# Kernel tuning notes

Hardware: AMD Instinct MI355X
Metric: run time of the kernel (lower is better)

The kernel has to match this reference:

```python
import jax, jax.numpy as jnp
import numpy as np

IN_C = 256
ATTN_C = IN_C // 8
B, H, W = 4, 64, 64


def setup_inputs() -> dict:
    key = jax.random.key(0)
    ks = jax.random.split(key, 8)
    x = jax.random.normal(ks[0], (B, IN_C, W, H), dtype=jnp.float32)
    # 1x1 convs == channel-mixing matmuls: weight [out_c, in_c], bias [out_c]
    sq = 1.0 / np.sqrt(IN_C)
    Wq = jax.random.normal(ks[1], (ATTN_C, IN_C), dtype=jnp.float32) * sq
    bq = jnp.zeros((ATTN_C,), dtype=jnp.float32)
    Wk = jax.random.normal(ks[2], (ATTN_C, IN_C), dtype=jnp.float32) * sq
    bk = jnp.zeros((ATTN_C,), dtype=jnp.float32)
    Wv = jax.random.normal(ks[3], (IN_C, IN_C), dtype=jnp.float32) * sq
    bv = jnp.zeros((IN_C,), dtype=jnp.float32)
    # gamma initialized to zeros in the torch module; use a nonzero value so
    # the attention path contributes to the output/gradients.
    gamma = jnp.full((1,), 0.5, dtype=jnp.float32)
    return {"x": x, "Wq": Wq, "bq": bq, "Wk": Wk, "bk": bk,
            "Wv": Wv, "bv": bv, "gamma": gamma}


def reference(x, Wq, bq, Wk, bk, Wv, bv, gamma):
    bs, c, w, h = x.shape
    n = w * h
    xf = x.reshape(bs, c, n)                                   # [B, C, N]
    q = jnp.einsum('ac,bcn->ban', Wq, xf) + bq[:, None]        # [B, A, N]
    k = jnp.einsum('ac,bcn->ban', Wk, xf) + bk[:, None]        # [B, A, N]
    v = jnp.einsum('oc,bcn->bon', Wv, xf) + bv[:, None]        # [B, C, N]
    # energy = query.transpose(1,2) @ key  -> energy[b,i,j] = sum_a q[b,a,i] k[b,a,j]
    energy = jnp.einsum('bai,baj->bij', q, k)                  # [B, N, N]
    # non-standard: softmax over dim=1 (the query/i axis)
    attn = jax.nn.softmax(energy, axis=1)
    # out = value @ attn.transpose(1,2) -> out[b,c,i] = sum_j v[b,c,j] attn[b,i,j]
    out = jnp.einsum('bcj,bij->bci', v, attn)                  # [B, C, N]
    out = out.reshape(bs, c, w, h)
    return gamma * out + x
```

## Files before the change

kernel.cpp:

```cpp
#include <hip/hip_runtime.h>

#define NBATCH 4
#define CIN 256
#define CATT 32
#define NPIX 4096

static constexpr float LOG2E_F = 1.4426950408889634f;

typedef __attribute__((ext_vector_type(8))) short bf16x8;
typedef __attribute__((ext_vector_type(4))) float f32x4;

__device__ __forceinline__ unsigned short f2bf_rne(float f) {
    unsigned u = __builtin_bit_cast(unsigned, f);
    return (unsigned short)((u + 0x7fffu + ((u >> 16) & 1u)) >> 16);
}
__device__ __forceinline__ float bf2f(unsigned short h) {
    unsigned u = (unsigned)h << 16;
    return __builtin_bit_cast(float, u);
}
__device__ __forceinline__ void split8(const float* p, bf16x8& hi, bf16x8& lo) {
    const float4 a = *reinterpret_cast<const float4*>(p);
    const float4 b = *reinterpret_cast<const float4*>(p + 4);
    const float f[8] = {a.x, a.y, a.z, a.w, b.x, b.y, b.z, b.w};
    #pragma unroll
    for (int e = 0; e < 8; ++e) {
        const unsigned short h = f2bf_rne(f[e]);
        hi[e] = (short)h;
        lo[e] = (short)f2bf_rne(f[e] - bf2f(h));
    }
}
__device__ __forceinline__ bf16x8 cvt8(const float* p) {
    const float4 a = *reinterpret_cast<const float4*>(p);
    const float4 b = *reinterpret_cast<const float4*>(p + 4);
    const float f[8] = {a.x, a.y, a.z, a.w, b.x, b.y, b.z, b.w};
    bf16x8 r;
    #pragma unroll
    for (int e = 0; e < 8; ++e) r[e] = (short)f2bf_rne(f[e]);
    return r;
}
__device__ __forceinline__ void gl_lds16(const unsigned short* g, unsigned short* l) {
    __builtin_amdgcn_global_load_lds(
        (const __attribute__((address_space(1))) unsigned int*)g,
        (__attribute__((address_space(3))) unsigned int*)l, 16, 0, 0);
}

__global__ __launch_bounds__(256, 2)
void transpose_kernel(const float* __restrict__ x, unsigned short* __restrict__ xT)
{
    __shared__ unsigned short sT[64][68];
    const int t = threadIdx.x;
    const int nblk = blockIdx.x * 64;
    const int cblk = blockIdx.y * 64;
    const int b = blockIdx.z;
    const float* xb = x + ((size_t)b * CIN + cblk) * NPIX + nblk;
    const int lc = t >> 2, ln = (t & 3) << 4;
    #pragma unroll
    for (int u = 0; u < 4; ++u) {
        const float4 v = *reinterpret_cast<const float4*>(&xb[(size_t)lc * NPIX + ln + 4 * u]);
        sT[ln + 4 * u + 0][lc] = f2bf_rne(v.x);
        sT[ln + 4 * u + 1][lc] = f2bf_rne(v.y);
        sT[ln + 4 * u + 2][lc] = f2bf_rne(v.z);
        sT[ln + 4 * u + 3][lc] = f2bf_rne(v.w);
    }
    __syncthreads();
    const int rn = t >> 2, cs = (t & 3) << 4;
    const uint2 d0 = *reinterpret_cast<const uint2*>(&sT[rn][cs + 0]);
    const uint2 d1 = *reinterpret_cast<const uint2*>(&sT[rn][cs + 4]);
    const uint2 d2 = *reinterpret_cast<const uint2*>(&sT[rn][cs + 8]);
    const uint2 d3 = *reinterpret_cast<const uint2*>(&sT[rn][cs + 12]);
    unsigned short* dst = xT + ((size_t)b * NPIX + nblk + rn) * CIN + cblk + cs;
    *reinterpret_cast<uint4*>(dst)     = make_uint4(d0.x, d0.y, d1.x, d1.y);
    *reinterpret_cast<uint4*>(dst + 8) = make_uint4(d2.x, d2.y, d3.x, d3.y);
}

__global__ __launch_bounds__(256, 2)
void proj_qk_kernel(const float* __restrict__ Wq, const float* __restrict__ bq,
                    const float* __restrict__ Wk, const float* __restrict__ bk,
                    const unsigned short* __restrict__ xT,
                    unsigned short* __restrict__ qt, unsigned short* __restrict__ kt)
{
    const int t = threadIdx.x, w = t >> 6, l = t & 63, lr = l & 15, lg = l >> 4;
    const int b = blockIdx.y;
    const int n0 = blockIdx.x * 64 + 16 * w;
    const unsigned short* xrow = xT + ((size_t)b * NPIX + n0 + lr) * CIN + lg * 8;
    f32x4 aq[2] = {{0.f,0.f,0.f,0.f},{0.f,0.f,0.f,0.f}};
    f32x4 ak2[2] = {{0.f,0.f,0.f,0.f},{0.f,0.f,0.f,0.f}};
    #pragma unroll
    for (int ks = 0; ks < 8; ++ks) {
        const int ko = ks * 32 + lg * 8;
        const bf16x8 bx = *reinterpret_cast<const bf16x8*>(xrow + ks * 32);
        #pragma unroll
        for (int mt = 0; mt < 2; ++mt) {
            bf16x8 wh, wl;
            split8(&Wq[(size_t)(mt * 16 + lr) * CIN + ko], wh, wl);
            aq[mt] = __builtin_amdgcn_mfma_f32_16x16x32_bf16(wh, bx, aq[mt], 0, 0, 0);
            aq[mt] = __builtin_amdgcn_mfma_f32_16x16x32_bf16(wl, bx, aq[mt], 0, 0, 0);
            split8(&Wk[(size_t)(mt * 16 + lr) * CIN + ko], wh, wl);
            ak2[mt] = __builtin_amdgcn_mfma_f32_16x16x32_bf16(wh, bx, ak2[mt], 0, 0, 0);
            ak2[mt] = __builtin_amdgcn_mfma_f32_16x16x32_bf16(wl, bx, ak2[mt], 0, 0, 0);
        }
    }
    #pragma unroll
    for (int mt = 0; mt < 2; ++mt) {
        const float4 b4q = *reinterpret_cast<const float4*>(&bq[16 * mt + (lg << 2)]);
        const float4 b4k = *reinterpret_cast<const float4*>(&bk[16 * mt + (lg << 2)]);
        ushort4 uq, uk;
        uq.x = f2bf_rne(LOG2E_F * (aq[mt][0] + b4q.x));
        uq.y = f2bf_rne(LOG2E_F * (aq[mt][1] + b4q.y));
        uq.z = f2bf_rne(LOG2E_F * (aq[mt][2] + b4q.z));
        uq.w = f2bf_rne(LOG2E_F * (aq[mt][3] + b4q.w));
        uk.x = f2bf_rne(ak2[mt][0] + b4k.x);
        uk.y = f2bf_rne(ak2[mt][1] + b4k.y);
        uk.z = f2bf_rne(ak2[mt][2] + b4k.z);
        uk.w = f2bf_rne(ak2[mt][3] + b4k.w);
        const size_t base = ((size_t)b * NPIX + n0 + lr) * CATT + 16 * mt + (lg << 2);
        *reinterpret_cast<ushort4*>(&qt[base]) = uq;
        *reinterpret_cast<ushort4*>(&kt[base]) = uk;
    }
}

__global__ __launch_bounds__(256, 2)
void stats_kernel(const unsigned short* __restrict__ qt,
                  const unsigned short* __restrict__ kt, float* __restrict__ rs)
{
    __shared__ float sred[4][16];
    const int n = blockIdx.x;
    const int b = n & 3;
    const int jblk = (n >> 2) * 32;
    const int t = threadIdx.x, w = t >> 6, l = t & 63, lr = l & 15, lg = l >> 4;
    const int jsl = w & 1;
    const int ih = w >> 1;
    const unsigned short* qb = qt + (size_t)b * NPIX * CATT;
    const unsigned short* kb = kt + (size_t)b * NPIX * CATT;

    const bf16x8 kfrag = *reinterpret_cast<const bf16x8*>(
        &kb[(size_t)(jblk + 16 * jsl + lr) * CATT + lg * 8]);
    const f32x4 zero = {0.f, 0.f, 0.f, 0.f};
    const unsigned short* qp = qb + (size_t)(ih * 2048 + lr) * CATT + lg * 8;

    float s0 = 0.f, s1 = 0.f, s2 = 0.f, s3 = 0.f;
    bf16x8 qc0 = *reinterpret_cast<const bf16x8*>(qp);
    bf16x8 qc1 = *reinterpret_cast<const bf16x8*>(qp + 16 * CATT);
    bf16x8 qc2 = *reinterpret_cast<const bf16x8*>(qp + 32 * CATT);
    bf16x8 qc3 = *reinterpret_cast<const bf16x8*>(qp + 48 * CATT);

    for (int ib = 0; ib < 2048; ib += 64) {
        bf16x8 qn0, qn1, qn2, qn3;
        const bool more = (ib + 64) < 2048;
        if (more) {
            const unsigned short* q2 = qp + (size_t)(ib + 64) * CATT;
            qn0 = *reinterpret_cast<const bf16x8*>(q2);
            qn1 = *reinterpret_cast<const bf16x8*>(q2 + 16 * CATT);
            qn2 = *reinterpret_cast<const bf16x8*>(q2 + 32 * CATT);
            qn3 = *reinterpret_cast<const bf16x8*>(q2 + 48 * CATT);
        }
        f32x4 d;
        d = __builtin_amdgcn_mfma_f32_16x16x32_bf16(kfrag, qc0, zero, 0, 0, 0);
        s0 += __builtin_amdgcn_exp2f(d[0]); s1 += __builtin_amdgcn_exp2f(d[1]);
        s2 += __builtin_amdgcn_exp2f(d[2]); s3 += __builtin_amdgcn_exp2f(d[3]);
        d = __builtin_amdgcn_mfma_f32_16x16x32_bf16(kfrag, qc1, zero, 0, 0, 0);
        s0 += __builtin_amdgcn_exp2f(d[0]); s1 += __builtin_amdgcn_exp2f(d[1]);
        s2 += __builtin_amdgcn_exp2f(d[2]); s3 += __builtin_amdgcn_exp2f(d[3]);
        d = __builtin_amdgcn_mfma_f32_16x16x32_bf16(kfrag, qc2, zero, 0, 0, 0);
        s0 += __builtin_amdgcn_exp2f(d[0]); s1 += __builtin_amdgcn_exp2f(d[1]);
        s2 += __builtin_amdgcn_exp2f(d[2]); s3 += __builtin_amdgcn_exp2f(d[3]);
        d = __builtin_amdgcn_mfma_f32_16x16x32_bf16(kfrag, qc3, zero, 0, 0, 0);
        s0 += __builtin_amdgcn_exp2f(d[0]); s1 += __builtin_amdgcn_exp2f(d[1]);
        s2 += __builtin_amdgcn_exp2f(d[2]); s3 += __builtin_amdgcn_exp2f(d[3]);
        if (more) { qc0 = qn0; qc1 = qn1; qc2 = qn2; qc3 = qn3; }
    }
    #pragma unroll
    for (int m = 1; m < 16; m <<= 1) {
        s0 += __shfl_xor(s0, m); s1 += __shfl_xor(s1, m);
        s2 += __shfl_xor(s2, m); s3 += __shfl_xor(s3, m);
    }
    if (lr == 0) {
        sred[w][(lg << 2) + 0] = s0;
        sred[w][(lg << 2) + 1] = s1;
        sred[w][(lg << 2) + 2] = s2;
        sred[w][(lg << 2) + 3] = s3;
    }
    __syncthreads();
    if (t < 32) {
        const int j16 = t & 15, js = t >> 4;
        const float s = sred[js][j16] + sred[js + 2][j16];
        rs[(size_t)b * NPIX + jblk + t] = 1.0f / s;
    }
}

__global__ __launch_bounds__(256, 2)
void proj_v_kernel(const float* __restrict__ Wv, const float* __restrict__ bv,
                   const unsigned short* __restrict__ xT, const float* __restrict__ rs,
                   const float* __restrict__ gamma, unsigned short* __restrict__ vt)
{
    const int t = threadIdx.x, w = t >> 6, l = t & 63, lr = l & 15, lg = l >> 4;
    const int b = blockIdx.y;
    const int n0 = blockIdx.x * 32;
    const int cb = 64 * w;
    const unsigned short* xa = xT + ((size_t)b * NPIX + n0) * CIN;
    f32x4 acc[2][4] = {};
    #pragma unroll
    for (int ks = 0; ks < 8; ++ks) {
        const int ko = ks * 32 + lg * 8;
        bf16x8 af[2];
        #pragma unroll
        for (int mt = 0; mt < 2; ++mt)
            af[mt] = *reinterpret_cast<const bf16x8*>(&xa[(size_t)(16 * mt + lr) * CIN + ko]);
        #pragma unroll
        for (int ct = 0; ct < 4; ++ct) {
            const bf16x8 wf = cvt8(&Wv[(size_t)(cb + 16 * ct + lr) * CIN + ko]);
            #pragma unroll
            for (int mt = 0; mt < 2; ++mt)
                acc[mt][ct] = __builtin_amdgcn_mfma_f32_16x16x32_bf16(af[mt], wf, acc[mt][ct], 0, 0, 0);
        }
    }
    const float gv = gamma[0];
    #pragma unroll
    for (int mt = 0; mt < 2; ++mt) {
        const int nr = n0 + 16 * mt + (lg << 2);
        const float4 rs4 = *reinterpret_cast<const float4*>(&rs[(size_t)b * NPIX + nr]);
        #pragma unroll
        for (int ct = 0; ct < 4; ++ct) {
            const int c = cb + 16 * ct + lr;
            const float bb = bv[c];
            ushort4 u;
            u.x = f2bf_rne(gv * rs4.x * (acc[mt][ct][0] + bb));
            u.y = f2bf_rne(gv * rs4.y * (acc[mt][ct][1] + bb));
            u.z = f2bf_rne(gv * rs4.z * (acc[mt][ct][2] + bb));
            u.w = f2bf_rne(gv * rs4.w * (acc[mt][ct][3] + bb));
            *reinterpret_cast<ushort4*>(&vt[((size_t)b * CIN + c) * NPIX + nr]) = u;
        }
    }
}

__global__ __launch_bounds__(256, 2)
void out_kernel(const unsigned short* __restrict__ qt,
                const unsigned short* __restrict__ kt,
                const unsigned short* __restrict__ vt,
                const float* __restrict__ x, float* __restrict__ out)
{
    __shared__ unsigned short sV[3][128 * 64];
    __shared__ unsigned short sK[2][64 * 32];
    __shared__ unsigned short sPl[2][64 * 64];
    const int n = blockIdx.x;
    const int b = n & 3;
    const int rest = n >> 2;
    const int ch = rest & 1;
    const int it = rest >> 1;
    const int iblk = it * 64;
    const int cblk = ch * 128;
    const int t = threadIdx.x, w = t >> 6, l = t & 63, lr = l & 15, lg = l >> 4;
    const unsigned short* qb = qt + (size_t)b * NPIX * CATT;
    const unsigned short* kb = kt + (size_t)b * NPIX * CATT;
    const unsigned short* vb = vt + (size_t)b * CIN * NPIX;
    const f32x4 zero = {0.f, 0.f, 0.f, 0.f};

    bf16x8 qfrag[4];
    #pragma unroll
    for (int nt = 0; nt < 4; ++nt)
        qfrag[nt] = *reinterpret_cast<const bf16x8*>(
            &qb[(size_t)(iblk + 16 * nt + lr) * CATT + lg * 8]);

    const unsigned short* vsrcq[4];
    #pragma unroll
    for (int q = 0; q < 4; ++q) {
        const int r = (4 * w + q) * 8 + (l >> 3);
        const int p = l & 7;
        vsrcq[q] = vb + (size_t)(cblk + r) * NPIX + ((p ^ (r & 7)) * 8);
    }
    const int rk = w * 16 + (l >> 2);
    const unsigned short* ksrc0 = kb + (size_t)rk * CATT + (((l & 3) ^ (rk & 3)) * 8);

    const int krow = 16 * w + lr;
    const int kbyte = krow * 64 + ((lg * 16) ^ ((krow & 3) << 4));
    const int cl0 = 32 * w + lr;
    const int cl1 = cl0 + 16;
    int vbyte[2][2];
    #pragma unroll
    for (int kk = 0; kk < 2; ++kk) {
        vbyte[0][kk] = cl0 * 128 + ((kk * 64 + lg * 16) ^ ((cl0 & 7) << 4));
        vbyte[1][kk] = cl1 * 128 + ((kk * 64 + lg * 16) ^ ((cl1 & 7) << 4));
    }
    const int swz = (lr & 7) << 4;
    const int wb0 = lr * 128 + (((16 * w + 4 * lg) * 2) ^ swz);
    const int rb_col0 = (16 * lg) ^ swz;
    const int rb_col1 = (64 + 16 * lg) ^ swz;

    f32x4 acc[2][4] = {};

    #pragma unroll
    for (int q = 0; q < 4; ++q) gl_lds16(vsrcq[q], &sV[0][(4 * w + q) * 512]);
    gl_lds16(ksrc0, &sK[0][w * 512]);
    __syncthreads();

    int vs_cur = 0;
    for (int jb = 0; jb < 64; ++jb) {
        const int vs_next = (vs_cur == 2) ? 0 : vs_cur + 1;
        const int vs_prev = (vs_cur == 0) ? 2 : vs_cur - 1;
        if (jb < 63) {
            const int jn = (jb + 1) * 64;
            #pragma unroll
            for (int q = 0; q < 4; ++q)
                gl_lds16(vsrcq[q] + jn, &sV[vs_next][(4 * w + q) * 512]);
            gl_lds16(ksrc0 + (size_t)jn * CATT, &sK[(jb + 1) & 1][w * 512]);
        }
        {
            const char* skp = reinterpret_cast<const char*>(&sK[jb & 1][0]);
            const bf16x8 kf = *reinterpret_cast<const bf16x8*>(skp + kbyte);
            char* spw = reinterpret_cast<char*>(&sPl[jb & 1][0]);
            #pragma unroll
            for (int nt = 0; nt < 4; ++nt) {
                const f32x4 e = __builtin_amdgcn_mfma_f32_16x16x32_bf16(kf, qfrag[nt], zero, 0, 0, 0);
                const float p0 = __builtin_amdgcn_exp2f(e[0]);
                const float p1 = __builtin_amdgcn_exp2f(e[1]);
                const float p2 = __builtin_amdgcn_exp2f(e[2]);
                const float p3 = __builtin_amdgcn_exp2f(e[3]);
                unsigned w0, w1;
                asm("v_cvt_pk_bf16_f32 %0, %1, %2" : "=v"(w0) : "v"(p0), "v"(p1));
                asm("v_cvt_pk_bf16_f32 %0, %1, %2" : "=v"(w1) : "v"(p2), "v"(p3));
                *reinterpret_cast<uint2*>(spw + wb0 + nt * 2048) = make_uint2(w0, w1);
            }
        }
        if (jb > 0) {
            const char* spr = reinterpret_cast<const char*>(&sPl[(jb - 1) & 1][0]);
            const char* svp = reinterpret_cast<const char*>(&sV[vs_prev][0]);
            #pragma unroll
            for (int kk = 0; kk < 2; ++kk) {
                const int rbc = (kk == 0) ? rb_col0 : rb_col1;
                bf16x8 pf[4];
                #pragma unroll
                for (int nt = 0; nt < 4; ++nt)
                    pf[nt] = *reinterpret_cast<const bf16x8*>(spr + lr * 128 + nt * 2048 + rbc);
                const bf16x8 v0 = *reinterpret_cast<const bf16x8*>(svp + vbyte[0][kk]);
                const bf16x8 v1 = *reinterpret_cast<const bf16x8*>(svp + vbyte[1][kk]);
                __builtin_amdgcn_s_setprio(1);
                #pragma unroll
                for (int nt = 0; nt < 4; ++nt) {
                    acc[0][nt] = __builtin_amdgcn_mfma_f32_16x16x32_bf16(v0, pf[nt], acc[0][nt], 0, 0, 0);
                    acc[1][nt] = __builtin_amdgcn_mfma_f32_16x16x32_bf16(v1, pf[nt], acc[1][nt], 0, 0, 0);
                }
                __builtin_amdgcn_s_setprio(0);
            }
        }
        __syncthreads();
        vs_cur = vs_next;
    }
    {
        const int vs_prev = (vs_cur == 0) ? 2 : vs_cur - 1;
        const char* spr = reinterpret_cast<const char*>(&sPl[1][0]);
        const char* svp = reinterpret_cast<const char*>(&sV[vs_prev][0]);
        #pragma unroll
        for (int kk = 0; kk < 2; ++kk) {
            const int rbc = (kk == 0) ? rb_col0 : rb_col1;
            bf16x8 pf[4];
            #pragma unroll
            for (int nt = 0; nt < 4; ++nt)
                pf[nt] = *reinterpret_cast<const bf16x8*>(spr + lr * 128 + nt * 2048 + rbc);
            const bf16x8 v0 = *reinterpret_cast<const bf16x8*>(svp + vbyte[0][kk]);
            const bf16x8 v1 = *reinterpret_cast<const bf16x8*>(svp + vbyte[1][kk]);
            #pragma unroll
            for (int nt = 0; nt < 4; ++nt) {
                acc[0][nt] = __builtin_amdgcn_mfma_f32_16x16x32_bf16(v0, pf[nt], acc[0][nt], 0, 0, 0);
                acc[1][nt] = __builtin_amdgcn_mfma_f32_16x16x32_bf16(v1, pf[nt], acc[1][nt], 0, 0, 0);
            }
        }
    }

    const float* xb = x + (size_t)b * CIN * NPIX;
    float* ob = out + (size_t)b * CIN * NPIX;
    #pragma unroll
    for (int mt = 0; mt < 2; ++mt)
        #pragma unroll
        for (int nt = 0; nt < 4; ++nt)
            #pragma unroll
            for (int r = 0; r < 4; ++r) {
                const int c = cblk + 32 * w + 16 * mt + (lg << 2) + r;
                const size_t idx = (size_t)c * NPIX + iblk + 16 * nt + lr;
                ob[idx] = acc[mt][nt][r] + xb[idx];
            }
}

extern "C" void kernel_launch(void* const* d_in, const int* in_sizes, int n_in,
                              void* d_out, int out_size, void* d_ws, size_t ws_size,
                              hipStream_t stream)
{
    const float* x     = (const float*)d_in[0];
    const float* Wq    = (const float*)d_in[1];
    const float* bq    = (const float*)d_in[2];
    const float* Wk    = (const float*)d_in[3];
    const float* bk    = (const float*)d_in[4];
    const float* Wv    = (const float*)d_in[5];
    const float* bv    = (const float*)d_in[6];
    const float* gamma = (const float*)d_in[7];
    float* out = (float*)d_out;

    unsigned short* xT = (unsigned short*)d_ws;
    unsigned short* qt = xT + (size_t)NBATCH * NPIX * CIN;
    unsigned short* kt = qt + (size_t)NBATCH * NPIX * CATT;
    unsigned short* vt = kt + (size_t)NBATCH * NPIX * CATT;
    float* rsw = (float*)(vt + (size_t)NBATCH * CIN * NPIX);

    transpose_kernel<<<dim3(NPIX / 64, CIN / 64, NBATCH), 256, 0, stream>>>(x, xT);
    proj_qk_kernel<<<dim3(NPIX / 64, NBATCH), 256, 0, stream>>>(Wq, bq, Wk, bk, xT, qt, kt);
    stats_kernel<<<dim3((NPIX / 32) * NBATCH), 256, 0, stream>>>(qt, kt, rsw);
    proj_v_kernel<<<dim3(NPIX / 32, NBATCH), 256, 0, stream>>>(Wv, bv, xT, rsw, gamma, vt);
    out_kernel<<<dim3((NPIX / 64) * 2 * NBATCH), 256, 0, stream>>>(qt, kt, vt, x, out);
}
```

Before: 128.3 us.

## Fuse Q/K/V projections into one kernel and apply softmax reciprocal in attention loop

Merges the QK and V projection kernels into a single launch: two waves compute Q/K for a 32-pixel tile while all four waves compute V. Because V no longer depends on the column-softmax normalizer, the reciprocal sums are applied to the exponentiated probabilities inside the attention loop instead. This saves one kernel launch and one pass over xT, at the cost of extra multiplies and a per-iteration global load of the normalizers in the hot loop, plus an unbalanced wave workload in the fused projection.

New measurement: 129.1 us. No clear change (+0.6%).

```diff
diff --git a/kernel.cpp b/kernel.cpp
--- a/kernel.cpp
+++ b/kernel.cpp
@@ -74,48 +74,90 @@
 }
 
 __global__ __launch_bounds__(256, 2)
-void proj_qk_kernel(const float* __restrict__ Wq, const float* __restrict__ bq,
-                    const float* __restrict__ Wk, const float* __restrict__ bk,
-                    const unsigned short* __restrict__ xT,
-                    unsigned short* __restrict__ qt, unsigned short* __restrict__ kt)
+void proj_fused_kernel(const float* __restrict__ Wq, const float* __restrict__ bq,
+                       const float* __restrict__ Wk, const float* __restrict__ bk,
+                       const float* __restrict__ Wv, const float* __restrict__ bv,
+                       const float* __restrict__ gamma,
+                       const unsigned short* __restrict__ xT,
+                       unsigned short* __restrict__ qt, unsigned short* __restrict__ kt,
+                       unsigned short* __restrict__ vt)
 {
     const int t = threadIdx.x, w = t >> 6, l = t & 63, lr = l & 15, lg = l >> 4;
     const int b = blockIdx.y;
-    const int n0 = blockIdx.x * 64 + 16 * w;
-    const unsigned short* xrow = xT + ((size_t)b * NPIX + n0 + lr) * CIN + lg * 8;
-    f32x4 aq[2] = {{0.f,0.f,0.f,0.f},{0.f,0.f,0.f,0.f}};
-    f32x4 ak2[2] = {{0.f,0.f,0.f,0.f},{0.f,0.f,0.f,0.f}};
+    const int n0 = blockIdx.x * 32;
+
+    if (w < 2) {
+        const int nq = n0 + 16 * w;
+        const unsigned short* xrow = xT + ((size_t)b * NPIX + nq + lr) * CIN + lg * 8;
+        f32x4 aq[2] = {{0.f,0.f,0.f,0.f},{0.f,0.f,0.f,0.f}};
+        f32x4 ak2[2] = {{0.f,0.f,0.f,0.f},{0.f,0.f,0.f,0.f}};
+        #pragma unroll
+        for (int ks = 0; ks < 8; ++ks) {
+            const int ko = ks * 32 + lg * 8;
+            const bf16x8 bx = *reinterpret_cast<const bf16x8*>(xrow + ks * 32);
+            #pragma unroll
+            for (int mt = 0; mt < 2; ++mt) {
+                bf16x8 wh, wl;
+                split8(&Wq[(size_t)(mt * 16 + lr) * CIN + ko], wh, wl);
+                aq[mt] = __builtin_amdgcn_mfma_f32_16x16x32_bf16(wh, bx, aq[mt], 0, 0, 0);
+                aq[mt] = __builtin_amdgcn_mfma_f32_16x16x32_bf16(wl, bx, aq[mt], 0, 0, 0);
+                split8(&Wk[(size_t)(mt * 16 + lr) * CIN + ko], wh, wl);
+                ak2[mt] = __builtin_amdgcn_mfma_f32_16x16x32_bf16(wh, bx, ak2[mt], 0, 0, 0);
+                ak2[mt] = __builtin_amdgcn_mfma_f32_16x16x32_bf16(wl, bx, ak2[mt], 0, 0, 0);
+            }
+        }
+        #pragma unroll
+        for (int mt = 0; mt < 2; ++mt) {
+            const float4 b4q = *reinterpret_cast<const float4*>(&bq[16 * mt + (lg << 2)]);
+            const float4 b4k = *reinterpret_cast<const float4*>(&bk[16 * mt + (lg << 2)]);
+            ushort4 uq, uk;
+            uq.x = f2bf_rne(LOG2E_F * (aq[mt][0] + b4q.x));
+            uq.y = f2bf_rne(LOG2E_F * (aq[mt][1] + b4q.y));
+            uq.z = f2bf_rne(LOG2E_F * (aq[mt][2] + b4q.z));
+            uq.w = f2bf_rne(LOG2E_F * (aq[mt][3] + b4q.w));
+            uk.x = f2bf_rne(ak2[mt][0] + b4k.x);
+            uk.y = f2bf_rne(ak2[mt][1] + b4k.y);
+            uk.z = f2bf_rne(ak2[mt][2] + b4k.z);
+            uk.w = f2bf_rne(ak2[mt][3] + b4k.w);
+            const size_t base = ((size_t)b * NPIX + nq + lr) * CATT + 16 * mt + (lg << 2);
+            *reinterpret_cast<ushort4*>(&qt[base]) = uq;
+            *reinterpret_cast<ushort4*>(&kt[base]) = uk;
+        }
+    }
+
+    const int cb = 64 * w;
+    const unsigned short* xa = xT + ((size_t)b * NPIX + n0) * CIN;
+    f32x4 acc[2][4] = {};
     #pragma unroll
     for (int ks = 0; ks < 8; ++ks) {
         const int ko = ks * 32 + lg * 8;
-        const bf16x8 bx = *reinterpret_cast<const bf16x8*>(xrow + ks * 32);
-        #pragma unroll
-        for (int mt = 0; mt < 2; ++mt) {
-            bf16x8 wh, wl;
-            split8(&Wq[(size_t)(mt * 16 + lr) * CIN + ko], wh, wl);
-            aq[mt] = __builtin_amdgcn_mfma_f32_16x16x32_bf16(wh, bx, aq[mt], 0, 0, 0);
-            aq[mt] = __builtin_amdgcn_mfma_f32_16x16x32_bf16(wl, bx, aq[mt], 0, 0, 0);
-            split8(&Wk[(size_t)(mt * 16 + lr) * CIN + ko], wh, wl);
-            ak2[mt] = __builtin_amdgcn_mfma_f32_16x16x32_bf16(wh, bx, ak2[mt], 0, 0, 0);
-            ak2[mt] = __builtin_amdgcn_mfma_f32_16x16x32_bf16(wl, bx, ak2[mt], 0, 0, 0);
-        }
-    }
+        bf16x8 af[2];
+        #pragma unroll
+        for (int mt = 0; mt < 2; ++mt)
+            af[mt] = *reinterpret_cast<const bf16x8*>(&xa[(size_t)(16 * mt + lr) * CIN + ko]);
+        #pragma unroll
+        for (int ct = 0; ct < 4; ++ct) {
+            const bf16x8 wf = cvt8(&Wv[(size_t)(cb + 16 * ct + lr) * CIN + ko]);
+            #pragma unroll
+            for (int mt = 0; mt < 2; ++mt)
+                acc[mt][ct] = __builtin_amdgcn_mfma_f32_16x16x32_bf16(af[mt], wf, acc[mt][ct], 0, 0, 0);
+        }
+    }
+    const float gv = gamma[0];
     #pragma unroll
     for (int mt = 0; mt < 2; ++mt) {
-        const float4 b4q = *reinterpret_cast<const float4*>(&bq[16 * mt + (lg << 2)]);
-        const float4 b4k = *reinterpret_cast<const float4*>(&bk[16 * mt + (lg << 2)]);
-        ushort4 uq, uk;
-        uq.x = f2bf_rne(LOG2E_F * (aq[mt][0] + b4q.x));
-        uq.y = f2bf_rne(LOG2E_F * (aq[mt][1] + b4q.y));
-        uq.z = f2bf_rne(LOG2E_F * (aq[mt][2] + b4q.z));
-        uq.w = f2bf_rne(LOG2E_F * (aq[mt][3] + b4q.w));
-        uk.x = f2bf_rne(ak2[mt][0] + b4k.x);
-        uk.y = f2bf_rne(ak2[mt][1] + b4k.y);
-        uk.z = f2bf_rne(ak2[mt][2] + b4k.z);
-        uk.w = f2bf_rne(ak2[mt][3] + b4k.w);
-        const size_t base = ((size_t)b * NPIX + n0 + lr) * CATT + 16 * mt + (lg << 2);
-        *reinterpret_cast<ushort4*>(&qt[base]) = uq;
-        *reinterpret_cast<ushort4*>(&kt[base]) = uk;
+        const int nr = n0 + 16 * mt + (lg << 2);
+        #pragma unroll
+        for (int ct = 0; ct < 4; ++ct) {
+            const int c = cb + 16 * ct + lr;
+            const float bb = bv[c];
+            ushort4 u;
+            u.x = f2bf_rne(gv * (acc[mt][ct][0] + bb));
+            u.y = f2bf_rne(gv * (acc[mt][ct][1] + bb));
+            u.z = f2bf_rne(gv * (acc[mt][ct][2] + bb));
+            u.w = f2bf_rne(gv * (acc[mt][ct][3] + bb));
+            *reinterpret_cast<ushort4*>(&vt[((size_t)b * CIN + c) * NPIX + nr]) = u;
+        }
     }
 }
 
@@ -189,54 +231,10 @@
 }
 
 __global__ __launch_bounds__(256, 2)
-void proj_v_kernel(const float* __restrict__ Wv, const float* __restrict__ bv,
-                   const unsigned short* __restrict__ xT, const float* __restrict__ rs,
-                   const float* __restrict__ gamma, unsigned short* __restrict__ vt)
-{
-    const int t = threadIdx.x, w = t >> 6, l = t & 63, lr = l & 15, lg = l >> 4;
-    const int b = blockIdx.y;
-    const int n0 = blockIdx.x * 32;
-    const int cb = 64 * w;
-    const unsigned short* xa = xT + ((size_t)b * NPIX + n0) * CIN;
-    f32x4 acc[2][4] = {};
-    #pragma unroll
-    for (int ks = 0; ks < 8; ++ks) {
-        const int ko = ks * 32 + lg * 8;
-        bf16x8 af[2];
-        #pragma unroll
-        for (int mt = 0; mt < 2; ++mt)
-            af[mt] = *reinterpret_cast<const bf16x8*>(&xa[(size_t)(16 * mt + lr) * CIN + ko]);
-        #pragma unroll
-        for (int ct = 0; ct < 4; ++ct) {
-            const bf16x8 wf = cvt8(&Wv[(size_t)(cb + 16 * ct + lr) * CIN + ko]);
-            #pragma unroll
-            for (int mt = 0; mt < 2; ++mt)
-                acc[mt][ct] = __builtin_amdgcn_mfma_f32_16x16x32_bf16(af[mt], wf, acc[mt][ct], 0, 0, 0);
-        }
-    }
-    const float gv = gamma[0];
-    #pragma unroll
-    for (int mt = 0; mt < 2; ++mt) {
-        const int nr = n0 + 16 * mt + (lg << 2);
-        const float4 rs4 = *reinterpret_cast<const float4*>(&rs[(size_t)b * NPIX + nr]);
-        #pragma unroll
-        for (int ct = 0; ct < 4; ++ct) {
-            const int c = cb + 16 * ct + lr;
-            const float bb = bv[c];
-            ushort4 u;
-            u.x = f2bf_rne(gv * rs4.x * (acc[mt][ct][0] + bb));
-            u.y = f2bf_rne(gv * rs4.y * (acc[mt][ct][1] + bb));
-            u.z = f2bf_rne(gv * rs4.z * (acc[mt][ct][2] + bb));
-            u.w = f2bf_rne(gv * rs4.w * (acc[mt][ct][3] + bb));
-            *reinterpret_cast<ushort4*>(&vt[((size_t)b * CIN + c) * NPIX + nr]) = u;
-        }
-    }
-}
-
-__global__ __launch_bounds__(256, 2)
 void out_kernel(const unsigned short* __restrict__ qt,
                 const unsigned short* __restrict__ kt,
                 const unsigned short* __restrict__ vt,
+                const float* __restrict__ rs,
                 const float* __restrict__ x, float* __restrict__ out)
 {
     __shared__ unsigned short sV[3][128 * 64];
@@ -253,6 +251,7 @@
     const unsigned short* qb = qt + (size_t)b * NPIX * CATT;
     const unsigned short* kb = kt + (size_t)b * NPIX * CATT;
     const unsigned short* vb = vt + (size_t)b * CIN * NPIX;
+    const float* rsb = rs + (size_t)b * NPIX;
     const f32x4 zero = {0.f, 0.f, 0.f, 0.f};
 
     bf16x8 qfrag[4];
@@ -308,13 +307,15 @@
             const char* skp = reinterpret_cast<const char*>(&sK[jb & 1][0]);
             const bf16x8 kf = *reinterpret_cast<const bf16x8*>(skp + kbyte);
             char* spw = reinterpret_cast<char*>(&sPl[jb & 1][0]);
+            const float4 r4 = *reinterpret_cast<const float4*>(
+                &rsb[jb * 64 + 16 * w + (lg << 2)]);
             #pragma unroll
             for (int nt = 0; nt < 4; ++nt) {
                 const f32x4 e = __builtin_amdgcn_mfma_f32_16x16x32_bf16(kf, qfrag[nt], zero, 0, 0, 0);
-                const float p0 = __builtin_amdgcn_exp2f(e[0]);
-                const float p1 = __builtin_amdgcn_exp2f(e[1]);
-                const float p2 = __builtin_amdgcn_exp2f(e[2]);
-                const float p3 = __builtin_amdgcn_exp2f(e[3]);
+                const float p0 = __builtin_amdgcn_exp2f(e[0]) * r4.x;
+                const float p1 = __builtin_amdgcn_exp2f(e[1]) * r4.y;
+                const float p2 = __builtin_amdgcn_exp2f(e[2]) * r4.z;
+                const float p3 = __builtin_amdgcn_exp2f(e[3]) * r4.w;
                 unsigned w0, w1;
                 asm("v_cvt_pk_bf16_f32 %0, %1, %2" : "=v"(w0) : "v"(p0), "v"(p1));
                 asm("v_cvt_pk_bf16_f32 %0, %1, %2" : "=v"(w1) : "v"(p2), "v"(p3));
@@ -401,8 +402,8 @@
     float* rsw = (float*)(vt + (size_t)NBATCH * CIN * NPIX);
 
     transpose_kernel<<<dim3(NPIX / 64, CIN / 64, NBATCH), 256, 0, stream>>>(x, xT);
-    proj_qk_kernel<<<dim3(NPIX / 64, NBATCH), 256, 0, stream>>>(Wq, bq, Wk, bk, xT, qt, kt);
+    proj_fused_kernel<<<dim3(NPIX / 32, NBATCH), 256, 0, stream>>>(
+        Wq, bq, Wk, bk, Wv, bv, gamma, xT, qt, kt, vt);
     stats_kernel<<<dim3((NPIX / 32) * NBATCH), 256, 0, stream>>>(qt, kt, rsw);
-    proj_v_kernel<<<dim3(NPIX / 32, NBATCH), 256, 0, stream>>>(Wv, bv, xT, rsw, gamma, vt);
-    out_kernel<<<dim3((NPIX / 64) * 2 * NBATCH), 256, 0, stream>>>(qt, kt, vt, x, out);
-}
+    out_kernel<<<dim3((NPIX / 64) * 2 * NBATCH), 256, 0, stream>>>(qt, kt, vt, rsw, x, out);
+}
```
